# Optimization experiments

Hardware: AMD Instinct MI355X
Metric: run time of the kernel (lower is better)

## Reference

```python
import jax, jax.numpy as jnp
import numpy as np
import math

B, T, C = 2, 1400, 256
H = 16
D = C // H            # 16
FF = 1024
VOCAB = 1400
SLOTS = 256
EPS = 1e-5


def _ln(x, g, b):
    m = jnp.mean(x, axis=-1, keepdims=True)
    v = jnp.mean(jnp.square(x - m), axis=-1, keepdims=True)
    return (x - m) * jax.lax.rsqrt(v + EPS) * g + b


def setup_inputs() -> dict:
    key = jax.random.key(0)
    ks = jax.random.split(key, 24)
    s = 0.02
    inp = {
        "x": jax.random.normal(ks[0], (B, T, C), dtype=jnp.float32),
        "disease_ids": jax.random.randint(ks[1], (B, T), 0, VOCAB),
        # nn.MultiheadAttention params (torch layout: [out,in])
        "in_proj_w": jax.random.normal(ks[2], (3 * C, C)) * s,
        "in_proj_b": jnp.zeros((3 * C,), jnp.float32),
        "out_proj_w": jax.random.normal(ks[3], (C, C)) * s,
        "out_proj_b": jnp.zeros((C,), jnp.float32),
        # LayerNorms
        "ln1_g": jnp.ones((C,), jnp.float32), "ln1_b": jnp.zeros((C,), jnp.float32),
        "ln2_g": jnp.ones((C,), jnp.float32), "ln2_b": jnp.zeros((C,), jnp.float32),
        "ln3_g": jnp.ones((C,), jnp.float32), "ln3_b": jnp.zeros((C,), jnp.float32),
        # DiseaseGraphAttention
        "gq_w": jax.random.normal(ks[4], (C, C)) * s, "gq_b": jnp.zeros((C,), jnp.float32),
        "gk_w": jax.random.normal(ks[5], (C, C)) * s, "gk_b": jnp.zeros((C,), jnp.float32),
        "gv_w": jax.random.normal(ks[6], (C, C)) * s, "gv_b": jnp.zeros((C,), jnp.float32),
        "go_w": jax.random.normal(ks[7], (C, C)) * s, "go_b": jnp.zeros((C,), jnp.float32),
        "affinity": jax.random.normal(ks[8], (VOCAB, VOCAB)) * 0.01,
        # LongTermMemoryBank (only the read path affects the returned output)
        "mem_bank": jax.random.normal(ks[9], (SLOTS, C)) * 0.1,
        "read_w": jax.random.normal(ks[10], (SLOTS, C)) * s,
        "read_b": jnp.zeros((SLOTS,), jnp.float32),
        # FFN
        "ffn_w1": jax.random.normal(ks[11], (FF, C)) * s, "ffn_b1": jnp.zeros((FF,), jnp.float32),
        "ffn_w2": jax.random.normal(ks[12], (C, FF)) * s, "ffn_b2": jnp.zeros((C,), jnp.float32),
    }
    return inp


def reference(x, disease_ids, in_proj_w, in_proj_b, out_proj_w, out_proj_b,
              ln1_g, ln1_b, ln2_g, ln2_b, ln3_g, ln3_b,
              gq_w, gq_b, gk_w, gk_b, gv_w, gv_b, go_w, go_b, affinity,
              mem_bank, read_w, read_b, ffn_w1, ffn_b1, ffn_w2, ffn_b2):
    scale = 1.0 / math.sqrt(D)

    # ---- standard MHA (pre-norm, residual), dropout in eval mode ----
    h = _ln(x, ln1_g, ln1_b)
    qkv = h @ in_proj_w.T + in_proj_b                      # [B,T,3C]
    q, k, v = jnp.split(qkv, 3, axis=-1)
    q = q.reshape(B, T, H, D); k = k.reshape(B, T, H, D); v = v.reshape(B, T, H, D)
    scores = jnp.einsum('bthd,bshd->bhts', q, k) * scale   # [B,H,T,T]
    attn = jax.nn.softmax(scores, axis=-1)
    o = jnp.einsum('bhts,bshd->bthd', attn, v).reshape(B, T, C)
    x = x + (o @ out_proj_w.T + out_proj_b)

    # ---- disease-graph attention with gathered affinity bias ----
    h = _ln(x, ln2_g, ln2_b)
    q = (h @ gq_w.T + gq_b).reshape(B, T, H, D)
    k = (h @ gk_w.T + gk_b).reshape(B, T, H, D)
    v = (h @ gv_w.T + gv_b).reshape(B, T, H, D)
    aff = affinity[disease_ids]                            # [B,T,VOCAB] (VOCAB == T)
    scores = jnp.einsum('bthd,bshd->bhts', q, k) * scale + aff[:, None, :, :] * 0.1
    attn = jax.nn.softmax(scores, axis=-1)
    o = jnp.einsum('bhts,bshd->bthd', attn, v).reshape(B, T, C)
    x = x + (o @ go_w.T + go_b)

    # ---- memory-bank read (write/erase only mutate params, not the output) ----
    read_weights = jax.nn.softmax(x @ read_w.T + read_b, axis=-1)   # [B,T,SLOTS]
    x = x + jnp.einsum('bts,sc->btc', read_weights, mem_bank)

    # ---- FFN ----
    h = _ln(x, ln3_g, ln3_b)
    ff = jax.nn.gelu(h @ ffn_w1.T + ffn_b1, approximate=False) @ ffn_w2.T + ffn_b2
    return x + ff
```

## Files before the change

kernel.cpp:

```cpp
#include <hip/hip_runtime.h>
#include <hip/hip_bf16.h>
#include <math.h>

namespace {

typedef __attribute__((ext_vector_type(4))) float f32x4;
typedef __attribute__((ext_vector_type(8))) short s16x8;
typedef __attribute__((ext_vector_type(4))) short s16x4;
typedef unsigned short ushort_t;

constexpr int kB = 2, kT = 1400, kC = 256, kH = 16, kFF = 1024;
constexpr int kBT = kB * kT;
constexpr float kEps = 1e-5f;
constexpr int kSP = 5;
constexpr int kSLen = 280;
constexpr int SBLK = 288;
constexpr int KPITCH = 24;
constexpr float kQScale   = 0.25f * 1.4426950408889634f;
constexpr float kAffScale = 0.1f * 1.4426950408889634f;

__device__ __forceinline__ ushort_t f2bf(float f) {
    unsigned u = __float_as_uint(f);
    u += 0x7fffu + ((u >> 16) & 1u);
    return (ushort_t)(u >> 16);
}
__device__ __forceinline__ float bf2f(ushort_t u) {
    return __uint_as_float(((unsigned)u) << 16);
}
__device__ __forceinline__ unsigned pk2bf(float a, float b) {
    __hip_bfloat162 t = __float22bfloat162_rn(make_float2(a, b));
    union { __hip_bfloat162 h; unsigned u; } cv; cv.h = t;
    return cv.u;
}
__device__ __forceinline__ float fast_exp2(float x) {
    float r;
    asm("v_exp_f32 %0, %1" : "=v"(r) : "v"(x));
    return r;
}

__global__ __launch_bounds__(256) void convert_kernel(
        const float* __restrict__ in_proj_w, const float* __restrict__ gq_w,
        const float* __restrict__ gk_w, const float* __restrict__ gv_w,
        const float* __restrict__ out_proj_w, const float* __restrict__ go_w,
        const float* __restrict__ ffn_w1, const float* __restrict__ ffn_w2,
        const float* __restrict__ read_w, const float* __restrict__ mem_bank,
        const float* __restrict__ gq_b, const float* __restrict__ gk_b,
        const float* __restrict__ gv_b,
        ushort_t* __restrict__ wdst, float* __restrict__ gqkvb) {
    const int bid = blockIdx.x, tid = threadIdx.x;
    if (bid == 608) {
        gqkvb[tid] = gq_b[tid];
        gqkvb[256 + tid] = gk_b[tid];
        gqkvb[512 + tid] = gv_b[tid];
        return;
    }
    const int u0 = (bid * 256 + tid) * 8;
    if (u0 >= 1114112) {
        #pragma unroll
        for (int j = 0; j < 8; j++) {
            const int d = u0 - 1114112 + j;
            wdst[1114112 + d] = f2bf(mem_bank[(d & 255) * 256 + (d >> 8)]);
        }
        return;
    }
    const float* src; int off;
    if      (u0 < 196608)  { src = in_proj_w;  off = u0; }
    else if (u0 < 262144)  { src = gq_w;       off = u0 - 196608; }
    else if (u0 < 327680)  { src = gk_w;       off = u0 - 262144; }
    else if (u0 < 393216)  { src = gv_w;       off = u0 - 327680; }
    else if (u0 < 458752)  { src = out_proj_w; off = u0 - 393216; }
    else if (u0 < 524288)  { src = go_w;       off = u0 - 458752; }
    else if (u0 < 786432)  { src = ffn_w1;     off = u0 - 524288; }
    else if (u0 < 1048576) { src = ffn_w2;     off = u0 - 786432; }
    else                   { src = read_w;     off = u0 - 1048576; }
    #pragma unroll
    for (int j = 0; j < 8; j++) wdst[u0 + j] = f2bf(src[off + j]);
}

__global__ __launch_bounds__(256) void ln_kernel(
        const float* __restrict__ x, const float* __restrict__ g,
        const float* __restrict__ b, ushort_t* __restrict__ out) {
    __shared__ float red[10];
    const int row = blockIdx.x, tid = threadIdx.x;
    const float v = x[row * kC + tid];
    float s1 = v, s2 = v * v;
    #pragma unroll
    for (int off = 32; off > 0; off >>= 1) {
        s1 += __shfl_down(s1, off);
        s2 += __shfl_down(s2, off);
    }
    if ((tid & 63) == 0) { red[tid >> 6] = s1; red[4 + (tid >> 6)] = s2; }
    __syncthreads();
    if (tid == 0) {
        red[8] = red[0] + red[1] + red[2] + red[3];
        red[9] = red[4] + red[5] + red[6] + red[7];
    }
    __syncthreads();
    const float mean = red[8] * (1.f / kC);
    const float var = red[9] * (1.f / kC) - mean * mean;
    out[row * kC + tid] = f2bf((v - mean) * rsqrtf(var + kEps) * g[tid] + b[tid]);
}

__global__ __launch_bounds__(256) void gemm16_kernel(
        const ushort_t* __restrict__ A, const ushort_t* __restrict__ W,
        const float* __restrict__ bias, const float* __restrict__ res,
        float* __restrict__ outf, ushort_t* __restrict__ outb,
        ushort_t* __restrict__ outK, ushort_t* __restrict__ outV,
        int M, int N, int K, int ldo, int act, int mode) {
    __shared__ ushort_t dsA[64 * 64];
    __shared__ ushort_t dsW[64 * 64];
    const int tid = threadIdx.x;
    const int lane = tid & 63, wave = tid >> 6;
    const int qi = lane & 15, g = lane >> 4;
    const int wm = (wave >> 1) * 32, wn = (wave & 1) * 32;
    const int m0 = blockIdx.x * 64, n0 = blockIdx.y * 64;

    f32x4 acc[2][2] = {};
    for (int kt = 0; kt < K; kt += 64) {
        __syncthreads();
        #pragma unroll
        for (int j = 0; j < 2; ++j) {
            const int u = tid + j * 256;
            const int row = u >> 3, c = u & 7;
            const int cs = c ^ (row & 7);
            const int gmA = min(m0 + row, M - 1);
            *(s16x8*)&dsA[row * 64 + cs * 8] =
                *(const s16x8*)&A[(size_t)gmA * K + kt + c * 8];
            *(s16x8*)&dsW[row * 64 + cs * 8] =
                *(const s16x8*)&W[(size_t)(n0 + row) * K + kt + c * 8];
        }
        __syncthreads();
        #pragma unroll
        for (int kk = 0; kk < 2; ++kk) {
            s16x8 af[2], bf[2];
            #pragma unroll
            for (int f = 0; f < 2; ++f) {
                const int r = wm + f * 16 + qi;
                af[f] = *(const s16x8*)&dsA[r * 64 + (((kk * 4 + g) ^ (r & 7)) * 8)];
            }
            #pragma unroll
            for (int nn = 0; nn < 2; ++nn) {
                const int r = wn + nn * 16 + qi;
                bf[nn] = *(const s16x8*)&dsW[r * 64 + (((kk * 4 + g) ^ (r & 7)) * 8)];
            }
            #pragma unroll
            for (int f = 0; f < 2; ++f)
                #pragma unroll
                for (int nn = 0; nn < 2; ++nn)
                    acc[f][nn] = __builtin_amdgcn_mfma_f32_16x16x32_bf16(
                        af[f], bf[nn], acc[f][nn], 0, 0, 0);
        }
    }
    #pragma unroll
    for (int f = 0; f < 2; ++f) {
        #pragma unroll
        for (int r = 0; r < 4; ++r) {
            const int gm = m0 + wm + f * 16 + g * 4 + r;
            if (gm >= M) continue;
            #pragma unroll
            for (int nn = 0; nn < 2; ++nn) {
                const int gn = n0 + wn + nn * 16 + qi;
                float v = acc[f][nn][r];
                if (bias) v += bias[gn];
                if (act == 1) v = 0.5f * v * (1.f + erff(v * 0.70710678f));
                if (res) v += res[(size_t)gm * ldo + gn];
                if (mode == 1) {
                    const int bb = (gm >= kT) ? 1 : 0;
                    const int ss = gm - bb * kT;
                    const int hh = (gn & 255) >> 4, dd = gn & 15;
                    const size_t hoff = (((size_t)(bb * 16 + hh)) * kT + ss) * 16 + dd;
                    if (gn < 256)      outb[hoff] = f2bf(v * kQScale);
                    else if (gn < 512) outK[hoff] = f2bf(v);
                    else               outV[hoff] = f2bf(v);
                } else {
                    if (outf) outf[(size_t)gm * ldo + gn] = v;
                    if (outb) outb[(size_t)gm * ldo + gn] = f2bf(v);
                }
            }
        }
    }
}

__global__ __launch_bounds__(256) void gemmcomb_kernel(
        const ushort_t* __restrict__ o_part, const float* __restrict__ l_part,
        const ushort_t* __restrict__ W, const float* __restrict__ bias,
        const float* __restrict__ res,
        const float* __restrict__ lng, const float* __restrict__ lnb,
        float* __restrict__ outf, ushort_t* __restrict__ outln) {
    __shared__ ushort_t dsA[16 * 256];
    __shared__ float ws1[4][16], ws2[4][16];
    const int tid = threadIdx.x;
    const int lane = tid & 63, wave = tid >> 6;
    const int qi = lane & 15, g = lane >> 4;
    const int wn = wave * 64;
    const int m0 = blockIdx.x * 16;

    {
        const int h = tid >> 4, r = tid & 15;
        const int gm = m0 + r;
        const int b = (gm >= kT) ? 1 : 0;
        const int t = gm - b * kT;
        float f[16] = {};
        float l = 0.f;
        #pragma unroll
        for (int p = 0; p < kSP; ++p) {
            const size_t sl_ = (size_t)((b * kSP + p) * 16 + h);
            l += l_part[sl_ * kT + t];
            const s16x8 v0 = *(const s16x8*)&o_part[(sl_ * kT + t) * 16];
            const s16x8 v1 = *(const s16x8*)&o_part[(sl_ * kT + t) * 16 + 8];
            #pragma unroll
            for (int j = 0; j < 8; j++) {
                f[j]     += bf2f((ushort_t)v0[j]);
                f[8 + j] += bf2f((ushort_t)v1[j]);
            }
        }
        const float li = 1.f / l;
        union { unsigned u4[4]; s16x8 s; } p0, p1;
        p0.u4[0] = pk2bf(f[0] * li, f[1] * li);
        p0.u4[1] = pk2bf(f[2] * li, f[3] * li);
        p0.u4[2] = pk2bf(f[4] * li, f[5] * li);
        p0.u4[3] = pk2bf(f[6] * li, f[7] * li);
        p1.u4[0] = pk2bf(f[8] * li, f[9] * li);
        p1.u4[1] = pk2bf(f[10] * li, f[11] * li);
        p1.u4[2] = pk2bf(f[12] * li, f[13] * li);
        p1.u4[3] = pk2bf(f[14] * li, f[15] * li);
        const int cg0 = h * 2, cg1 = h * 2 + 1;
        *(s16x8*)&dsA[r * 256 + ((cg0 ^ (r & 7)) << 3)] = p0.s;
        *(s16x8*)&dsA[r * 256 + ((cg1 ^ (r & 7)) << 3)] = p1.s;
    }
    __syncthreads();
    f32x4 acc[4] = {};
    for (int kt = 0; kt < 8; ++kt) {
        const int cg = kt * 4 + g;
        const s16x8 af = *(const s16x8*)&dsA[qi * 256 + ((cg ^ (qi & 7)) << 3)];
        #pragma unroll
        for (int nn = 0; nn < 4; ++nn) {
            const int wr = wn + nn * 16 + qi;
            const s16x8 bf = *(const s16x8*)&W[(size_t)wr * 256 + kt * 32 + g * 8];
            acc[nn] = __builtin_amdgcn_mfma_f32_16x16x32_bf16(af, bf, acc[nn], 0, 0, 0);
        }
    }
    float v[4][4];
    float s1[4] = {0.f, 0.f, 0.f, 0.f}, s2[4] = {0.f, 0.f, 0.f, 0.f};
    #pragma unroll
    for (int nn = 0; nn < 4; ++nn) {
        #pragma unroll
        for (int r = 0; r < 4; ++r) {
            const int row = 4 * g + r, col = wn + nn * 16 + qi;
            const size_t idx = (size_t)(m0 + row) * 256 + col;
            const float t = acc[nn][r] + bias[col] + res[idx];
            outf[idx] = t;
            v[nn][r] = t;
            s1[r] += t; s2[r] += t * t;
        }
    }
    if (outln) {
        #pragma unroll
        for (int r = 0; r < 4; ++r) {
            s1[r] += __shfl_xor(s1[r], 1); s2[r] += __shfl_xor(s2[r], 1);
            s1[r] += __shfl_xor(s1[r], 2); s2[r] += __shfl_xor(s2[r], 2);
            s1[r] += __shfl_xor(s1[r], 4); s2[r] += __shfl_xor(s2[r], 4);
            s1[r] += __shfl_xor(s1[r], 8); s2[r] += __shfl_xor(s2[r], 8);
        }
        if (qi == 0) {
            #pragma unroll
            for (int r = 0; r < 4; ++r) { ws1[wave][4 * g + r] = s1[r]; ws2[wave][4 * g + r] = s2[r]; }
        }
        __syncthreads();
        #pragma unroll
        for (int r = 0; r < 4; ++r) {
            const int row = 4 * g + r;
            const float S1 = ws1[0][row] + ws1[1][row] + ws1[2][row] + ws1[3][row];
            const float S2 = ws2[0][row] + ws2[1][row] + ws2[2][row] + ws2[3][row];
            const float mean = S1 * (1.f / 256.f);
            const float rstd = rsqrtf(S2 * (1.f / 256.f) - mean * mean + kEps);
            #pragma unroll
            for (int nn = 0; nn < 4; ++nn) {
                const int col = wn + nn * 16 + qi;
                outln[(size_t)(m0 + row) * 256 + col] =
                    f2bf((v[nn][r] - mean) * rstd * lng[col] + lnb[col]);
            }
        }
    }
}

__global__ __launch_bounds__(256) void memread_kernel(
        const float* __restrict__ x2, const ushort_t* __restrict__ wRead,
        const float* __restrict__ read_b, const ushort_t* __restrict__ wMemT,
        const float* __restrict__ lng, const float* __restrict__ lnb,
        float* __restrict__ xout, ushort_t* __restrict__ outln) {
    __shared__ ushort_t dsP[16 * 256];
    __shared__ float lsum[4][16];
    __shared__ float lt[16];
    __shared__ float ws1[4][16], ws2[4][16];
    const int tid = threadIdx.x;
    const int lane = tid & 63, wave = tid >> 6;
    const int qi = lane & 15, g = lane >> 4;
    const int wn = wave * 64;
    const int m0 = blockIdx.x * 16;

    {
        const int r = tid >> 4, e = tid & 15;
        const float* xr = x2 + (size_t)(m0 + r) * 256 + e * 16;
        #pragma unroll
        for (int i = 0; i < 2; i++) {
            const float4 va = *(const float4*)&xr[i * 8];
            const float4 vb = *(const float4*)&xr[i * 8 + 4];
            union { unsigned u4[4]; s16x8 s; } pu;
            pu.u4[0] = pk2bf(va.x, va.y);
            pu.u4[1] = pk2bf(va.z, va.w);
            pu.u4[2] = pk2bf(vb.x, vb.y);
            pu.u4[3] = pk2bf(vb.z, vb.w);
            const int cg = e * 2 + i;
            *(s16x8*)&dsP[r * 256 + ((cg ^ (r & 7)) << 3)] = pu.s;
        }
    }
    __syncthreads();
    f32x4 acc[4] = {};
    for (int kt = 0; kt < 8; ++kt) {
        const int cg = kt * 4 + g;
        const s16x8 af = *(const s16x8*)&dsP[qi * 256 + ((cg ^ (qi & 7)) << 3)];
        #pragma unroll
        for (int nn = 0; nn < 4; ++nn) {
            const int wr = wn + nn * 16 + qi;
            const s16x8 bf = *(const s16x8*)&wRead[(size_t)wr * 256 + kt * 32 + g * 8];
            acc[nn] = __builtin_amdgcn_mfma_f32_16x16x32_bf16(af, bf, acc[nn], 0, 0, 0);
        }
    }
    float p[4][4];
    float rs[4] = {0.f, 0.f, 0.f, 0.f};
    #pragma unroll
    for (int nn = 0; nn < 4; ++nn) {
        const float bb = read_b[wn + nn * 16 + qi];
        #pragma unroll
        for (int r = 0; r < 4; ++r) {
            p[nn][r] = __expf(acc[nn][r] + bb);
            rs[r] += p[nn][r];
        }
    }
    #pragma unroll
    for (int r = 0; r < 4; ++r) {
        rs[r] += __shfl_xor(rs[r], 1);
        rs[r] += __shfl_xor(rs[r], 2);
        rs[r] += __shfl_xor(rs[r], 4);
        rs[r] += __shfl_xor(rs[r], 8);
    }
    __syncthreads();
    if (qi == 0) {
        #pragma unroll
        for (int r = 0; r < 4; ++r) lsum[wave][4 * g + r] = rs[r];
    }
    #pragma unroll
    for (int nn = 0; nn < 4; ++nn) {
        #pragma unroll
        for (int r = 0; r < 4; ++r) {
            const int row = 4 * g + r, col = wn + nn * 16 + qi;
            const int cg = col >> 3, e = col & 7;
            dsP[row * 256 + ((cg ^ (row & 7)) << 3) + e] = f2bf(p[nn][r]);
        }
    }
    __syncthreads();
    if (tid < 16)
        lt[tid] = 1.f / (lsum[0][tid] + lsum[1][tid] + lsum[2][tid] + lsum[3][tid]);
    __syncthreads();
    f32x4 acc2[4] = {};
    for (int kt = 0; kt < 8; ++kt) {
        const int cg = kt * 4 + g;
        const s16x8 af = *(const s16x8*)&dsP[qi * 256 + ((cg ^ (qi & 7)) << 3)];
        #pragma unroll
        for (int nn = 0; nn < 4; ++nn) {
            const int wr = wn + nn * 16 + qi;
            const s16x8 bf = *(const s16x8*)&wMemT[(size_t)wr * 256 + kt * 32 + g * 8];
            acc2[nn] = __builtin_amdgcn_mfma_f32_16x16x32_bf16(af, bf, acc2[nn], 0, 0, 0);
        }
    }
    float xo[4][4];
    float s1[4] = {0.f, 0.f, 0.f, 0.f}, s2[4] = {0.f, 0.f, 0.f, 0.f};
    #pragma unroll
    for (int nn = 0; nn < 4; ++nn) {
        #pragma unroll
        for (int r = 0; r < 4; ++r) {
            const int row = 4 * g + r;
            const size_t idx = (size_t)(m0 + row) * 256 + wn + nn * 16 + qi;
            const float t = acc2[nn][r] * lt[row] + x2[idx];
            xout[idx] = t;
            xo[nn][r] = t;
            s1[r] += t; s2[r] += t * t;
        }
    }
    #pragma unroll
    for (int r = 0; r < 4; ++r) {
        s1[r] += __shfl_xor(s1[r], 1); s2[r] += __shfl_xor(s2[r], 1);
        s1[r] += __shfl_xor(s1[r], 2); s2[r] += __shfl_xor(s2[r], 2);
        s1[r] += __shfl_xor(s1[r], 4); s2[r] += __shfl_xor(s2[r], 4);
        s1[r] += __shfl_xor(s1[r], 8); s2[r] += __shfl_xor(s2[r], 8);
    }
    if (qi == 0) {
        #pragma unroll
        for (int r = 0; r < 4; ++r) { ws1[wave][4 * g + r] = s1[r]; ws2[wave][4 * g + r] = s2[r]; }
    }
    __syncthreads();
    #pragma unroll
    for (int r = 0; r < 4; ++r) {
        const int row = 4 * g + r;
        const float S1 = ws1[0][row] + ws1[1][row] + ws1[2][row] + ws1[3][row];
        const float S2 = ws2[0][row] + ws2[1][row] + ws2[2][row] + ws2[3][row];
        const float mean = S1 * (1.f / 256.f);
        const float rstd = rsqrtf(S2 * (1.f / 256.f) - mean * mean + kEps);
        #pragma unroll
        for (int nn = 0; nn < 4; ++nn) {
            const int col = wn + nn * 16 + qi;
            outln[(size_t)(m0 + row) * 256 + col] =
                f2bf((xo[nn][r] - mean) * rstd * lng[col] + lnb[col]);
        }
    }
}

template <bool kAff>
__global__ __launch_bounds__(512) void attn_mfma_kernel(
        const ushort_t* __restrict__ q, const ushort_t* __restrict__ kbuf,
        const ushort_t* __restrict__ vbuf, ushort_t* __restrict__ o_part,
        float* __restrict__ l_part,
        const float* __restrict__ affinity, const int* __restrict__ did) {
    __shared__ ushort_t ldsK[SBLK * KPITCH];
    __shared__ ushort_t ldsV[SBLK * 16];
    const int tid  = threadIdx.x;
    const int bid  = blockIdx.x;
    const int w    = (bid & 7) * 220 + (bid >> 3);
    const int slice = w / 11;
    const int ttile = w - slice * 11;
    const int h    = slice & 15;
    const int z    = slice >> 4;
    const int b    = (z >= 5) ? 1 : 0;
    const int sp   = z - b * 5;
    const int t0   = ttile * 128;
    const int s0   = sp * kSLen;
    const int lane = tid & 63;
    const int wave = tid >> 6;
    const int g    = lane >> 4;
    const int qi   = lane & 15;

    const int tq  = t0 + wave * 16 + qi;
    const int tqc = min(tq, kT - 1);
    const ushort_t* qhb = q + (size_t)(b * 16 + h) * kT * 16;
    s16x8 qb = {0, 0, 0, 0, 0, 0, 0, 0};
    if (g < 2) qb = *(const s16x8*)&qhb[(size_t)tqc * 16 + g * 8];
    const float* ar = nullptr;
    if (kAff) ar = affinity + (size_t)did[b * kT + tqc] * kT;

    const ushort_t* kb  = kbuf + (size_t)(b * 16 + h) * kT * 16;
    const ushort_t* vbp = vbuf + (size_t)(b * 16 + h) * kT * 16;
    for (int i = tid; i < SBLK * 2; i += 512) {
        const int sl = i >> 1, hf = i & 1;
        const int sg = min(s0 + sl, kT - 1);
        *(s16x8*)&ldsK[sl * KPITCH + hf * 8] =
            *(const s16x8*)&kb[(size_t)sg * 16 + hf * 8];
        *(s16x8*)&ldsV[sl * 16 + hf * 8] =
            *(const s16x8*)&vbp[(size_t)sg * 16 + hf * 8];
    }
    __syncthreads();

    f32x4 acc = {0.f, 0.f, 0.f, 0.f};
    float lrun = 0.f;
    const unsigned vaddr = (unsigned)(size_t)(&ldsV[0]) + lane * 8;
    s16x4 va0, va1;
    asm volatile("ds_read_b64_tr_b16 %0, %2\n\t"
                 "ds_read_b64_tr_b16 %1, %2 offset:512"
                 : "=&v"(va0), "=&v"(va1) : "v"(vaddr));

    #pragma unroll
    for (int c = 0; c < SBLK / 32; ++c) {
        const int sl0 = c * 32;
        const bool tail = (c == 8);
        const s16x8 ka0 = *(const s16x8*)&ldsK[(sl0 + qi) * KPITCH + (g & 1) * 8];
        const s16x8 ka1 = *(const s16x8*)&ldsK[(sl0 + 16 + qi) * KPITCH + (g & 1) * 8];
        const f32x4 z4 = {0.f, 0.f, 0.f, 0.f};
        f32x4 d0 = __builtin_amdgcn_mfma_f32_16x16x32_bf16(ka0, qb, z4, 0, 0, 0);
        f32x4 d1 = __builtin_amdgcn_mfma_f32_16x16x32_bf16(ka1, qb, z4, 0, 0, 0);
        float sv[8];
        #pragma unroll
        for (int r = 0; r < 4; r++) { sv[r] = d0[r]; sv[4 + r] = d1[r]; }
        if (kAff) {
            if (!tail) {
                const float4 a0 = *(const float4*)&ar[s0 + sl0 + 4 * g];
                const float4 a1 = *(const float4*)&ar[s0 + sl0 + 16 + 4 * g];
                sv[0] += kAffScale * a0.x; sv[1] += kAffScale * a0.y;
                sv[2] += kAffScale * a0.z; sv[3] += kAffScale * a0.w;
                sv[4] += kAffScale * a1.x; sv[5] += kAffScale * a1.y;
                sv[6] += kAffScale * a1.z; sv[7] += kAffScale * a1.w;
            } else {
                #pragma unroll
                for (int jj = 0; jj < 8; jj++) {
                    const int s_ = s0 + sl0 + 16 * (jj >> 2) + 4 * g + (jj & 3);
                    sv[jj] += kAffScale * ar[min(s_, kT - 1)];
                }
            }
        }
        float pv[8];
        #pragma unroll
        for (int jj = 0; jj < 8; jj++) pv[jj] = fast_exp2(sv[jj]);
        if (tail && g >= 2) { pv[4] = 0.f; pv[5] = 0.f; pv[6] = 0.f; pv[7] = 0.f; }
        lrun += ((pv[0] + pv[1]) + (pv[2] + pv[3])) + ((pv[4] + pv[5]) + (pv[6] + pv[7]));
        union { unsigned u[4]; s16x8 s; } pu;
        pu.u[0] = pk2bf(pv[0], pv[1]);
        pu.u[1] = pk2bf(pv[2], pv[3]);
        pu.u[2] = pk2bf(pv[4], pv[5]);
        pu.u[3] = pk2bf(pv[6], pv[7]);
        asm volatile("s_waitcnt lgkmcnt(0)" ::: "memory");
        __builtin_amdgcn_sched_barrier(0);
        s16x8 af;
        #pragma unroll
        for (int j = 0; j < 4; j++) { af[j] = va0[j]; af[4 + j] = va1[j]; }
        acc = __builtin_amdgcn_mfma_f32_16x16x32_bf16(af, pu.s, acc, 0, 0, 0);
        if (c < SBLK / 32 - 1) {
            asm volatile("ds_read_b64_tr_b16 %0, %2\n\t"
                         "ds_read_b64_tr_b16 %1, %2 offset:512"
                         : "=&v"(va0), "=&v"(va1) : "v"(vaddr + (sl0 + 32) * 32));
        }
    }
    lrun += __shfl_xor(lrun, 16);
    lrun += __shfl_xor(lrun, 32);
    const int slice_id = (b * kSP + sp) * 16 + h;
    if (lane < 16 && tq < kT)
        l_part[(size_t)slice_id * kT + tq] = lrun;
    ushort_t* ob = o_part + (size_t)slice_id * kT * 16;
    s16x4 ov;
    #pragma unroll
    for (int r = 0; r < 4; r++) ov[r] = (short)f2bf(acc[r]);
    if (tq < kT) *(s16x4*)&ob[(size_t)tq * 16 + 4 * g] = ov;
}

}

extern "C" void kernel_launch(void* const* d_in, const int* in_sizes, int n_in,
                              void* d_out, int out_size, void* d_ws, size_t ws_size,
                              hipStream_t stream) {
    const float* x          = (const float*)d_in[0];
    const int*   did        = (const int*)d_in[1];
    const float* in_proj_w  = (const float*)d_in[2];
    const float* in_proj_b  = (const float*)d_in[3];
    const float* out_proj_w = (const float*)d_in[4];
    const float* out_proj_b = (const float*)d_in[5];
    const float* ln1_g = (const float*)d_in[6];
    const float* ln1_b = (const float*)d_in[7];
    const float* ln2_g = (const float*)d_in[8];
    const float* ln2_b = (const float*)d_in[9];
    const float* ln3_g = (const float*)d_in[10];
    const float* ln3_b = (const float*)d_in[11];
    const float* gq_w = (const float*)d_in[12];
    const float* gq_b = (const float*)d_in[13];
    const float* gk_w = (const float*)d_in[14];
    const float* gk_b = (const float*)d_in[15];
    const float* gv_w = (const float*)d_in[16];
    const float* gv_b = (const float*)d_in[17];
    const float* go_w = (const float*)d_in[18];
    const float* go_b = (const float*)d_in[19];
    const float* affinity = (const float*)d_in[20];
    const float* mem_bank = (const float*)d_in[21];
    const float* read_w   = (const float*)d_in[22];
    const float* read_b   = (const float*)d_in[23];
    const float* ffn_w1 = (const float*)d_in[24];
    const float* ffn_b1 = (const float*)d_in[25];
    const float* ffn_w2 = (const float*)d_in[26];
    const float* ffn_b2 = (const float*)d_in[27];

    char* wsb = (char*)d_ws;
    ushort_t* o_part  = (ushort_t*)(wsb + 0);
    float*    l_part  = (float*)(wsb + 7168000);
    ushort_t* ff116   = (ushort_t*)(wsb + 8064000);
    float*    bufD    = (float*)(wsb + 13798400);
    ushort_t* bufA16  = (ushort_t*)(wsb + 16665600);
    float*    bufD2   = (float*)(wsb + 18099200);
    ushort_t* bufQ16  = (ushort_t*)(wsb + 20966400);
    ushort_t* bufK16  = (ushort_t*)(wsb + 22400000);
    ushort_t* bufV16  = (ushort_t*)(wsb + 23833600);
    ushort_t* wdst    = (ushort_t*)(wsb + 26700800);
    float*    gqkvb   = (float*)(wsb + 29191168);

    const ushort_t* wQKV1 = wdst;
    const ushort_t* wG    = wdst + 196608;
    const ushort_t* wO    = wdst + 393216;
    const ushort_t* wGO   = wdst + 458752;
    const ushort_t* wF1   = wdst + 524288;
    const ushort_t* wF2   = wdst + 786432;
    const ushort_t* wRead = wdst + 1048576;
    const ushort_t* wMemT = wdst + 1114112;

    const dim3 blk(256);
    const int MT = (kBT + 63) / 64;
    const dim3 g_qkv(MT, 12), g_c(MT, 4), g_ff(MT, 16);
    const dim3 g_at(11 * kH * kB * kSP);

    convert_kernel<<<609, blk, 0, stream>>>(in_proj_w, gq_w, gk_w, gv_w, out_proj_w,
                                            go_w, ffn_w1, ffn_w2, read_w, mem_bank,
                                            gq_b, gk_b, gv_b, wdst, gqkvb);
    ln_kernel<<<kBT, blk, 0, stream>>>(x, ln1_g, ln1_b, bufA16);
    gemm16_kernel<<<g_qkv, blk, 0, stream>>>(bufA16, wQKV1, in_proj_b, nullptr,
                                             nullptr, bufQ16, bufK16, bufV16,
                                             kBT, 768, kC, 768, 0, 1);
    attn_mfma_kernel<false><<<g_at, dim3(512), 0, stream>>>(bufQ16, bufK16, bufV16,
                                                            o_part, l_part,
                                                            nullptr, nullptr);
    gemmcomb_kernel<<<kBT / 16, blk, 0, stream>>>(o_part, l_part, wO, out_proj_b,
                                                  x, ln2_g, ln2_b, bufD2, bufA16);
    gemm16_kernel<<<g_qkv, blk, 0, stream>>>(bufA16, wG, gqkvb, nullptr,
                                             nullptr, bufQ16, bufK16, bufV16,
                                             kBT, 768, kC, 768, 0, 1);
    attn_mfma_kernel<true><<<g_at, dim3(512), 0, stream>>>(bufQ16, bufK16, bufV16,
                                                           o_part, l_part,
                                                           affinity, did);
    gemmcomb_kernel<<<kBT / 16, blk, 0, stream>>>(o_part, l_part, wGO, go_b,
                                                  bufD2, nullptr, nullptr,
                                                  bufD, nullptr);
    memread_kernel<<<kBT / 16, blk, 0, stream>>>(bufD, wRead, read_b, wMemT,
                                                 ln3_g, ln3_b, bufD, bufA16);
    gemm16_kernel<<<g_ff, blk, 0, stream>>>(bufA16, wF1, ffn_b1, nullptr,
                                            nullptr, ff116, nullptr, nullptr,
                                            kBT, kFF, kC, kFF, 1, 0);
    gemm16_kernel<<<g_c, blk, 0, stream>>>(ff116, wF2, ffn_b2, bufD,
                                           (float*)d_out, nullptr, nullptr, nullptr,
                                           kBT, kC, kFF, kC, 0, 0);
}
```

Before: 143.8 us.

## Fuse LayerNorm into QKV projection and merge FFN GEMMs into one kernel

Replaces the standalone LayerNorm and tiled 64x64 GEMM with a row-block kernel that computes LN1 in registers and performs the full QKV projection per 16-row block, reading weights directly from global memory. The two FFN GEMMs are fused into one kernel that keeps the GELU intermediate in shared memory, so the bf16 FF buffer round trip and two launches are removed. In exchange, each block streams the entire weight matrix from global/L2 without LDS staging, and there are fewer, larger blocks (175), which may cut parallelism and raise register pressure.

```diff
diff --git a/kernel.cpp b/kernel.cpp
--- a/kernel.cpp
+++ b/kernel.cpp
@@ -77,106 +77,180 @@
     for (int j = 0; j < 8; j++) wdst[u0 + j] = f2bf(src[off + j]);
 }
 
-__global__ __launch_bounds__(256) void ln_kernel(
-        const float* __restrict__ x, const float* __restrict__ g,
-        const float* __restrict__ b, ushort_t* __restrict__ out) {
-    __shared__ float red[10];
-    const int row = blockIdx.x, tid = threadIdx.x;
-    const float v = x[row * kC + tid];
-    float s1 = v, s2 = v * v;
-    #pragma unroll
-    for (int off = 32; off > 0; off >>= 1) {
-        s1 += __shfl_down(s1, off);
-        s2 += __shfl_down(s2, off);
-    }
-    if ((tid & 63) == 0) { red[tid >> 6] = s1; red[4 + (tid >> 6)] = s2; }
-    __syncthreads();
-    if (tid == 0) {
-        red[8] = red[0] + red[1] + red[2] + red[3];
-        red[9] = red[4] + red[5] + red[6] + red[7];
-    }
-    __syncthreads();
-    const float mean = red[8] * (1.f / kC);
-    const float var = red[9] * (1.f / kC) - mean * mean;
-    out[row * kC + tid] = f2bf((v - mean) * rsqrtf(var + kEps) * g[tid] + b[tid]);
-}
-
-__global__ __launch_bounds__(256) void gemm16_kernel(
-        const ushort_t* __restrict__ A, const ushort_t* __restrict__ W,
-        const float* __restrict__ bias, const float* __restrict__ res,
-        float* __restrict__ outf, ushort_t* __restrict__ outb,
-        ushort_t* __restrict__ outK, ushort_t* __restrict__ outV,
-        int M, int N, int K, int ldo, int act, int mode) {
-    __shared__ ushort_t dsA[64 * 64];
-    __shared__ ushort_t dsW[64 * 64];
+__global__ __launch_bounds__(256) void qkvln_kernel(
+        const float* __restrict__ xin, const ushort_t* __restrict__ hin,
+        const float* __restrict__ lng, const float* __restrict__ lnb,
+        const ushort_t* __restrict__ W, const float* __restrict__ bias,
+        ushort_t* __restrict__ outQ, ushort_t* __restrict__ outK,
+        ushort_t* __restrict__ outV) {
+    __shared__ ushort_t dsA[16 * 256];
     const int tid = threadIdx.x;
     const int lane = tid & 63, wave = tid >> 6;
     const int qi = lane & 15, g = lane >> 4;
-    const int wm = (wave >> 1) * 32, wn = (wave & 1) * 32;
-    const int m0 = blockIdx.x * 64, n0 = blockIdx.y * 64;
-
-    f32x4 acc[2][2] = {};
-    for (int kt = 0; kt < K; kt += 64) {
-        __syncthreads();
-        #pragma unroll
-        for (int j = 0; j < 2; ++j) {
-            const int u = tid + j * 256;
-            const int row = u >> 3, c = u & 7;
-            const int cs = c ^ (row & 7);
-            const int gmA = min(m0 + row, M - 1);
-            *(s16x8*)&dsA[row * 64 + cs * 8] =
-                *(const s16x8*)&A[(size_t)gmA * K + kt + c * 8];
-            *(s16x8*)&dsW[row * 64 + cs * 8] =
-                *(const s16x8*)&W[(size_t)(n0 + row) * K + kt + c * 8];
-        }
-        __syncthreads();
-        #pragma unroll
-        for (int kk = 0; kk < 2; ++kk) {
-            s16x8 af[2], bf[2];
+    const int m0 = blockIdx.x * 16;
+
+    if (xin) {
+        const int r = tid >> 4, e = tid & 15;
+        const float* xr = xin + (size_t)(m0 + r) * 256 + e * 16;
+        const float4 v0 = *(const float4*)&xr[0];
+        const float4 v1 = *(const float4*)&xr[4];
+        const float4 v2 = *(const float4*)&xr[8];
+        const float4 v3 = *(const float4*)&xr[12];
+        float s1 = ((v0.x + v0.y) + (v0.z + v0.w)) + ((v1.x + v1.y) + (v1.z + v1.w))
+                 + ((v2.x + v2.y) + (v2.z + v2.w)) + ((v3.x + v3.y) + (v3.z + v3.w));
+        float s2 = ((v0.x * v0.x + v0.y * v0.y) + (v0.z * v0.z + v0.w * v0.w))
+                 + ((v1.x * v1.x + v1.y * v1.y) + (v1.z * v1.z + v1.w * v1.w))
+                 + ((v2.x * v2.x + v2.y * v2.y) + (v2.z * v2.z + v2.w * v2.w))
+                 + ((v3.x * v3.x + v3.y * v3.y) + (v3.z * v3.z + v3.w * v3.w));
+        s1 += __shfl_xor(s1, 1); s2 += __shfl_xor(s2, 1);
+        s1 += __shfl_xor(s1, 2); s2 += __shfl_xor(s2, 2);
+        s1 += __shfl_xor(s1, 4); s2 += __shfl_xor(s2, 4);
+        s1 += __shfl_xor(s1, 8); s2 += __shfl_xor(s2, 8);
+        const float mean = s1 * (1.f / 256.f);
+        const float rstd = rsqrtf(s2 * (1.f / 256.f) - mean * mean + kEps);
+        const int c0 = e * 16;
+        const float4 ga = *(const float4*)&lng[c0];
+        const float4 gb = *(const float4*)&lng[c0 + 4];
+        const float4 gc = *(const float4*)&lng[c0 + 8];
+        const float4 gd = *(const float4*)&lng[c0 + 12];
+        const float4 ba = *(const float4*)&lnb[c0];
+        const float4 bb = *(const float4*)&lnb[c0 + 4];
+        const float4 bc = *(const float4*)&lnb[c0 + 8];
+        const float4 bd = *(const float4*)&lnb[c0 + 12];
+        union { unsigned u4[4]; s16x8 s; } p0, p1;
+        p0.u4[0] = pk2bf((v0.x - mean) * rstd * ga.x + ba.x,
+                         (v0.y - mean) * rstd * ga.y + ba.y);
+        p0.u4[1] = pk2bf((v0.z - mean) * rstd * ga.z + ba.z,
+                         (v0.w - mean) * rstd * ga.w + ba.w);
+        p0.u4[2] = pk2bf((v1.x - mean) * rstd * gb.x + bb.x,
+                         (v1.y - mean) * rstd * gb.y + bb.y);
+        p0.u4[3] = pk2bf((v1.z - mean) * rstd * gb.z + bb.z,
+                         (v1.w - mean) * rstd * gb.w + bb.w);
+        p1.u4[0] = pk2bf((v2.x - mean) * rstd * gc.x + bc.x,
+                         (v2.y - mean) * rstd * gc.y + bc.y);
+        p1.u4[1] = pk2bf((v2.z - mean) * rstd * gc.z + bc.z,
+                         (v2.w - mean) * rstd * gc.w + bc.w);
+        p1.u4[2] = pk2bf((v3.x - mean) * rstd * gd.x + bd.x,
+                         (v3.y - mean) * rstd * gd.y + bd.y);
+        p1.u4[3] = pk2bf((v3.z - mean) * rstd * gd.z + bd.z,
+                         (v3.w - mean) * rstd * gd.w + bd.w);
+        const int cg0 = e * 2, cg1 = e * 2 + 1;
+        *(s16x8*)&dsA[r * 256 + ((cg0 ^ (r & 7)) << 3)] = p0.s;
+        *(s16x8*)&dsA[r * 256 + ((cg1 ^ (r & 7)) << 3)] = p1.s;
+    } else {
+        const int r = tid >> 4, e = tid & 15;
+        const ushort_t* hr = hin + (size_t)(m0 + r) * 256 + e * 16;
+        #pragma unroll
+        for (int i = 0; i < 2; i++) {
+            const s16x8 v = *(const s16x8*)&hr[i * 8];
+            const int cg = e * 2 + i;
+            *(s16x8*)&dsA[r * 256 + ((cg ^ (r & 7)) << 3)] = v;
+        }
+    }
+    __syncthreads();
+    f32x4 acc[12] = {};
+    const int cbase = wave * 192;
+    for (int kt = 0; kt < 8; ++kt) {
+        const int cg = kt * 4 + g;
+        const s16x8 af = *(const s16x8*)&dsA[qi * 256 + ((cg ^ (qi & 7)) << 3)];
+        #pragma unroll
+        for (int nn = 0; nn < 12; ++nn) {
+            const int wr = cbase + nn * 16 + qi;
+            const s16x8 bf = *(const s16x8*)&W[(size_t)wr * 256 + kt * 32 + g * 8];
+            acc[nn] = __builtin_amdgcn_mfma_f32_16x16x32_bf16(af, bf, acc[nn], 0, 0, 0);
+        }
+    }
+    #pragma unroll
+    for (int nn = 0; nn < 12; ++nn) {
+        const int col = cbase + nn * 16 + qi;
+        const float bv = bias[col];
+        const int hh = (col & 255) >> 4, dd = col & 15;
+        #pragma unroll
+        for (int r = 0; r < 4; ++r) {
+            const int gm = m0 + 4 * g + r;
+            const int b = (gm >= kT) ? 1 : 0;
+            const int ss = gm - b * kT;
+            const size_t hoff = (((size_t)(b * 16 + hh)) * kT + ss) * 16 + dd;
+            const float v = acc[nn][r] + bv;
+            if (col < 256)      outQ[hoff] = f2bf(v * kQScale);
+            else if (col < 512) outK[hoff] = f2bf(v);
+            else                outV[hoff] = f2bf(v);
+        }
+    }
+}
+
+__global__ __launch_bounds__(256) void ffn_kernel(
+        const ushort_t* __restrict__ hin, const ushort_t* __restrict__ wF1,
+        const float* __restrict__ b1, const ushort_t* __restrict__ wF2,
+        const float* __restrict__ b2, const float* __restrict__ x3,
+        float* __restrict__ out) {
+    __shared__ ushort_t dsH[16 * 256];
+    __shared__ ushort_t dsF[16 * 1024];
+    const int tid = threadIdx.x;
+    const int lane = tid & 63, wave = tid >> 6;
+    const int qi = lane & 15, g = lane >> 4;
+    const int wn = wave * 64;
+    const int m0 = blockIdx.x * 16;
+
+    {
+        const int r = tid >> 4, e = tid & 15;
+        const ushort_t* hr = hin + (size_t)(m0 + r) * 256 + e * 16;
+        #pragma unroll
+        for (int i = 0; i < 2; i++) {
+            const s16x8 v = *(const s16x8*)&hr[i * 8];
+            const int cg = e * 2 + i;
+            *(s16x8*)&dsH[r * 256 + ((cg ^ (r & 7)) << 3)] = v;
+        }
+    }
+    __syncthreads();
+    #pragma unroll
+    for (int cc = 0; cc < 4; ++cc) {
+        f32x4 acc[4] = {};
+        for (int kt = 0; kt < 8; ++kt) {
+            const int cg = kt * 4 + g;
+            const s16x8 af = *(const s16x8*)&dsH[qi * 256 + ((cg ^ (qi & 7)) << 3)];
             #pragma unroll
-            for (int f = 0; f < 2; ++f) {
-                const int r = wm + f * 16 + qi;
-                af[f] = *(const s16x8*)&dsA[r * 64 + (((kk * 4 + g) ^ (r & 7)) * 8)];
+            for (int nn = 0; nn < 4; ++nn) {
+                const int wr = cc * 256 + wn + nn * 16 + qi;
+                const s16x8 bf = *(const s16x8*)&wF1[(size_t)wr * 256 + kt * 32 + g * 8];
+                acc[nn] = __builtin_amdgcn_mfma_f32_16x16x32_bf16(af, bf, acc[nn], 0, 0, 0);
             }
+        }
+        #pragma unroll
+        for (int nn = 0; nn < 4; ++nn) {
+            const int col = cc * 256 + wn + nn * 16 + qi;
+            const float bv = b1[col];
             #pragma unroll
-            for (int nn = 0; nn < 2; ++nn) {
-                const int r = wn + nn * 16 + qi;
-                bf[nn] = *(const s16x8*)&dsW[r * 64 + (((kk * 4 + g) ^ (r & 7)) * 8)];
+            for (int r = 0; r < 4; ++r) {
+                const int row = 4 * g + r;
+                float v = acc[nn][r] + bv;
+                v = 0.5f * v * (1.f + erff(v * 0.70710678f));
+                const int cg = col >> 3, e = col & 7;
+                dsF[row * 1024 + ((cg ^ (row & 7)) << 3) + e] = f2bf(v);
             }
-            #pragma unroll
-            for (int f = 0; f < 2; ++f)
-                #pragma unroll
-                for (int nn = 0; nn < 2; ++nn)
-                    acc[f][nn] = __builtin_amdgcn_mfma_f32_16x16x32_bf16(
-                        af[f], bf[nn], acc[f][nn], 0, 0, 0);
-        }
-    }
-    #pragma unroll
-    for (int f = 0; f < 2; ++f) {
-        #pragma unroll
-        for (int r = 0; r < 4; ++r) {
-            const int gm = m0 + wm + f * 16 + g * 4 + r;
-            if (gm >= M) continue;
-            #pragma unroll
-            for (int nn = 0; nn < 2; ++nn) {
-                const int gn = n0 + wn + nn * 16 + qi;
-                float v = acc[f][nn][r];
-                if (bias) v += bias[gn];
-                if (act == 1) v = 0.5f * v * (1.f + erff(v * 0.70710678f));
-                if (res) v += res[(size_t)gm * ldo + gn];
-                if (mode == 1) {
-                    const int bb = (gm >= kT) ? 1 : 0;
-                    const int ss = gm - bb * kT;
-                    const int hh = (gn & 255) >> 4, dd = gn & 15;
-                    const size_t hoff = (((size_t)(bb * 16 + hh)) * kT + ss) * 16 + dd;
-                    if (gn < 256)      outb[hoff] = f2bf(v * kQScale);
-                    else if (gn < 512) outK[hoff] = f2bf(v);
-                    else               outV[hoff] = f2bf(v);
-                } else {
-                    if (outf) outf[(size_t)gm * ldo + gn] = v;
-                    if (outb) outb[(size_t)gm * ldo + gn] = f2bf(v);
-                }
-            }
+        }
+    }
+    __syncthreads();
+    f32x4 acc2[4] = {};
+    for (int kt = 0; kt < 32; ++kt) {
+        const int cg = kt * 4 + g;
+        const s16x8 af = *(const s16x8*)&dsF[qi * 1024 + ((cg ^ (qi & 7)) << 3)];
+        #pragma unroll
+        for (int nn = 0; nn < 4; ++nn) {
+            const int wr = wn + nn * 16 + qi;
+            const s16x8 bf = *(const s16x8*)&wF2[(size_t)wr * 1024 + kt * 32 + g * 8];
+            acc2[nn] = __builtin_amdgcn_mfma_f32_16x16x32_bf16(af, bf, acc2[nn], 0, 0, 0);
+        }
+    }
+    #pragma unroll
+    for (int nn = 0; nn < 4; ++nn) {
+        const int col = wn + nn * 16 + qi;
+        const float bv = b2[col];
+        #pragma unroll
+        for (int r = 0; r < 4; ++r) {
+            const int row = 4 * g + r;
+            const size_t idx = (size_t)(m0 + row) * 256 + col;
+            out[idx] = acc2[nn][r] + bv + x3[idx];
         }
     }
 }
@@ -567,7 +641,6 @@
     char* wsb = (char*)d_ws;
     ushort_t* o_part  = (ushort_t*)(wsb + 0);
     float*    l_part  = (float*)(wsb + 7168000);
-    ushort_t* ff116   = (ushort_t*)(wsb + 8064000);
     float*    bufD    = (float*)(wsb + 13798400);
     ushort_t* bufA16  = (ushort_t*)(wsb + 16665600);
     float*    bufD2   = (float*)(wsb + 18099200);
@@ -587,37 +660,31 @@
     const ushort_t* wMemT = wdst + 1114112;
 
     const dim3 blk(256);
-    const int MT = (kBT + 63) / 64;
-    const dim3 g_qkv(MT, 12), g_c(MT, 4), g_ff(MT, 16);
+    const dim3 g_row(kBT / 16);
     const dim3 g_at(11 * kH * kB * kSP);
 
     convert_kernel<<<609, blk, 0, stream>>>(in_proj_w, gq_w, gk_w, gv_w, out_proj_w,
                                             go_w, ffn_w1, ffn_w2, read_w, mem_bank,
                                             gq_b, gk_b, gv_b, wdst, gqkvb);
-    ln_kernel<<<kBT, blk, 0, stream>>>(x, ln1_g, ln1_b, bufA16);
-    gemm16_kernel<<<g_qkv, blk, 0, stream>>>(bufA16, wQKV1, in_proj_b, nullptr,
-                                             nullptr, bufQ16, bufK16, bufV16,
-                                             kBT, 768, kC, 768, 0, 1);
+    qkvln_kernel<<<g_row, blk, 0, stream>>>(x, nullptr, ln1_g, ln1_b,
+                                            wQKV1, in_proj_b,
+                                            bufQ16, bufK16, bufV16);
     attn_mfma_kernel<false><<<g_at, dim3(512), 0, stream>>>(bufQ16, bufK16, bufV16,
                                                             o_part, l_part,
                                                             nullptr, nullptr);
-    gemmcomb_kernel<<<kBT / 16, blk, 0, stream>>>(o_part, l_part, wO, out_proj_b,
-                                                  x, ln2_g, ln2_b, bufD2, bufA16);
-    gemm16_kernel<<<g_qkv, blk, 0, stream>>>(bufA16, wG, gqkvb, nullptr,
-                                             nullptr, bufQ16, bufK16, bufV16,
-                                             kBT, 768, kC, 768, 0, 1);
+    gemmcomb_kernel<<<g_row, blk, 0, stream>>>(o_part, l_part, wO, out_proj_b,
+                                               x, ln2_g, ln2_b, bufD2, bufA16);
+    qkvln_kernel<<<g_row, blk, 0, stream>>>(nullptr, bufA16, nullptr, nullptr,
+                                            wG, gqkvb,
+                                            bufQ16, bufK16, bufV16);
     attn_mfma_kernel<true><<<g_at, dim3(512), 0, stream>>>(bufQ16, bufK16, bufV16,
                                                            o_part, l_part,
                                                            affinity, did);
-    gemmcomb_kernel<<<kBT / 16, blk, 0, stream>>>(o_part, l_part, wGO, go_b,
-                                                  bufD2, nullptr, nullptr,
-                                                  bufD, nullptr);
-    memread_kernel<<<kBT / 16, blk, 0, stream>>>(bufD, wRead, read_b, wMemT,
-                                                 ln3_g, ln3_b, bufD, bufA16);
-    gemm16_kernel<<<g_ff, blk, 0, stream>>>(bufA16, wF1, ffn_b1, nullptr,
-                                            nullptr, ff116, nullptr, nullptr,
-                                            kBT, kFF, kC, kFF, 1, 0);
-    gemm16_kernel<<<g_c, blk, 0, stream>>>(ff116, wF2, ffn_b2, bufD,
-                                           (float*)d_out, nullptr, nullptr, nullptr,
-                                           kBT, kC, kFF, kC, 0, 0);
-}
+    gemmcomb_kernel<<<g_row, blk, 0, stream>>>(o_part, l_part, wGO, go_b,
+                                               bufD2, nullptr, nullptr,
+                                               bufD, nullptr);
+    memread_kernel<<<g_row, blk, 0, stream>>>(bufD, wRead, read_b, wMemT,
+                                              ln3_g, ln3_b, bufD, bufA16);
+    ffn_kernel<<<g_row, blk, 0, stream>>>(bufA16, wF1, ffn_b1, wF2, ffn_b2,
+                                          bufD, (float*)d_out);
+}
```

After: 174.2 us. 1.21x slower.
